# Kernel optimization log

Hardware: AMD Instinct MI355X
Metric: run time of the kernel (lower is better)

The kernel has to match this reference:

```python
import jax, jax.numpy as jnp
import numpy as np

B, SQ, SKV, D = 16, 2048, 2048, 128


def setup_inputs() -> dict:
    key = jax.random.key(0)
    kq, kk, kv = jax.random.split(key, 3)
    q = jax.random.normal(kq, (B, SQ, D), dtype=jnp.float32)
    k = jax.random.normal(kk, (B, SKV, D), dtype=jnp.float32)
    v = jax.random.normal(kv, (B, SKV, D), dtype=jnp.float32)
    return {"q": q, "k": k, "v": v, "dropout_p": 0}


def reference(q, k, v, dropout_p):
    # scores = q @ k^T, scaled by 1/sqrt(d)
    scale = 1.0 / np.sqrt(q.shape[-1]).astype(np.float32)
    scores = jnp.einsum('bqd,bkd->bqk', q, k) * scale  # [B, SQ, SKV]
    attn = jax.nn.softmax(scores, axis=-1)
    # dropout with p=dropout_p (0 here -> identity; deterministic baseline)
    if dropout_p > 0:
        keep = 1.0 - dropout_p
        mask = jax.random.bernoulli(jax.random.key(42), keep, attn.shape)
        attn = jnp.where(mask, attn / keep, 0.0)
    return jnp.einsum('bqk,bkd->bqd', attn, v)
```

## Files before the change

### kernel.cpp

```cpp
#include <hip/hip_runtime.h>
#include <hip/hip_bf16.h>
#include <cstdint>
#include <cmath>

#define SQL 2048
#define SKVL 2048
#define DD 128
#define NB 16
#define QBLK 32
#define KVB 32
#define NT (SKVL / KVB)

typedef __attribute__((ext_vector_type(8))) short short8;
typedef __attribute__((ext_vector_type(4))) float f32x4;

__device__ __forceinline__ ushort f2bf(float x) {
    union { float f; uint32_t u; } v; v.f = x;
    uint32_t r = v.u + 0x7FFFu + ((v.u >> 16) & 1u);
    return (ushort)(r >> 16);
}

__global__ void convert_scale_k(const float* __restrict__ in, ushort* __restrict__ out, float scale) {
    size_t i = (size_t)blockIdx.x * blockDim.x + threadIdx.x;
    const f32x4* p = (const f32x4*)in + i * 2;
    f32x4 a = p[0], b = p[1];
    short8 o;
    o[0] = (short)f2bf(a[0] * scale);
    o[1] = (short)f2bf(a[1] * scale);
    o[2] = (short)f2bf(a[2] * scale);
    o[3] = (short)f2bf(a[3] * scale);
    o[4] = (short)f2bf(b[0] * scale);
    o[5] = (short)f2bf(b[1] * scale);
    o[6] = (short)f2bf(b[2] * scale);
    o[7] = (short)f2bf(b[3] * scale);
    *((short8*)out + i) = o;
}

__global__ void convert_k_tiled(const float* __restrict__ in, ushort* __restrict__ out) {
    int gid = blockIdx.x * blockDim.x + threadIdx.x;
    int c16 = gid & 15;
    int rg  = gid >> 4;
    int r   = rg & 31;
    int tile = rg >> 5;
    const f32x4* p = (const f32x4*)(in + (size_t)rg * DD + c16 * 8);
    f32x4 a = p[0], b = p[1];
    short8 o;
    o[0] = (short)f2bf(a[0]); o[1] = (short)f2bf(a[1]);
    o[2] = (short)f2bf(a[2]); o[3] = (short)f2bf(a[3]);
    o[4] = (short)f2bf(b[0]); o[5] = (short)f2bf(b[1]);
    o[6] = (short)f2bf(b[2]); o[7] = (short)f2bf(b[3]);
    int cs = c16 ^ (r & 7);
    *(short8*)(out + ((size_t)tile << 12) + r * 128 + cs * 8) = o;
}

__global__ void convert_vt_tiled(const float* __restrict__ v, ushort* __restrict__ vt) {
    __shared__ float tile[32][129];
    int bid = blockIdx.x;
    int kt = bid & 63;
    int b  = bid >> 6;
    int tx = threadIdx.x;
    const float* src = v + ((size_t)b * SKVL + (size_t)kt * 32) * DD;
#pragma unroll
    for (int i = 0; i < 16; ++i) {
        int e = i * 256 + tx;
        tile[e >> 7][e & 127] = src[e];
    }
    __syncthreads();
    ushort* dst = vt + ((size_t)bid << 12);
#pragma unroll
    for (int i = 0; i < 2; ++i) {
        int q = i * 256 + tx;
        int d = q >> 2;
        int csp = q & 3;
        int cs = csp ^ ((d >> 1) & 3);
        short8 o;
#pragma unroll
        for (int j = 0; j < 8; ++j) {
            int kv = (j >> 2) * 16 + cs * 4 + (j & 3);
            o[j] = (short)f2bf(tile[kv][d]);
        }
        *(short8*)(dst + d * 32 + csp * 8) = o;
    }
}

#define GLD_LDS16(gsrc, ldst) \
    __builtin_amdgcn_global_load_lds((const __attribute__((address_space(1))) uint32_t*)(gsrc), \
                                     (__attribute__((address_space(3))) uint32_t*)(ldst), 16, 0, 0)

__global__ __launch_bounds__(128, 2) void fattn(
    const ushort* __restrict__ qb, const ushort* __restrict__ kbt,
    const ushort* __restrict__ vbt, float* __restrict__ out)
{
    __shared__ short8 kls[2][512];
    __shared__ short8 vls[2][512];

    int bid = blockIdx.x;
    int swz = (bid & 7) * 128 + (bid >> 3);
    int b  = swz >> 6;
    int qt = swz & 63;
    int lane = threadIdx.x & 63;
    int w = threadIdx.x >> 6;
    int g = lane >> 4;
    int qi = lane & 15;
    int rx = qi & 7;
    int vx = g ^ ((qi >> 1) & 3);
    int qrow = qt * QBLK + w * 16 + qi;

    const ushort* ktile0 = kbt + ((size_t)(b * NT) << 12);
    const ushort* vtile0 = vbt + ((size_t)(b * NT) << 12);

    const ushort* qptr = qb + ((size_t)b * SQL + qrow) * DD;
    short8 qf[4];
#pragma unroll
    for (int ks = 0; ks < 4; ++ks)
        qf[ks] = *(const short8*)(qptr + ks * 32 + g * 8);

    f32x4 acc[8];
#pragma unroll
    for (int i = 0; i < 8; ++i) acc[i] = (f32x4)0.f;
    float m = -1e30f, lsum = 0.f;

#pragma unroll
    for (int i = 0; i < 4; ++i) {
        int off = w * 4096 + i * 1024;
        GLD_LDS16((const char*)ktile0 + off + lane * 16, (char*)&kls[0][0] + off);
        GLD_LDS16((const char*)vtile0 + off + lane * 16, (char*)&vls[0][0] + off);
    }
    __syncthreads();

    for (int t = 0; t < NT; ++t) {
        int cur = t & 1, nxt = cur ^ 1;
        if (t + 1 < NT) {
            const char* ks = (const char*)ktile0 + ((size_t)(t + 1) << 13);
            const char* vs = (const char*)vtile0 + ((size_t)(t + 1) << 13);
#pragma unroll
            for (int i = 0; i < 4; ++i) {
                int off = w * 4096 + i * 1024;
                GLD_LDS16(ks + off + lane * 16, (char*)&kls[nxt][0] + off);
                GLD_LDS16(vs + off + lane * 16, (char*)&vls[nxt][0] + off);
            }
        }
        f32x4 st[2];
        __builtin_amdgcn_s_setprio(1);
#pragma unroll
        for (int sub = 0; sub < 2; ++sub) {
            f32x4 s = (f32x4)0.f;
            int r = sub * 16 + qi;
#pragma unroll
            for (int ks = 0; ks < 4; ++ks) {
                short8 kf = kls[cur][r * 16 + ((ks * 4 + g) ^ rx)];
                s = __builtin_amdgcn_mfma_f32_16x16x32_bf16(kf, qf[ks], s, 0, 0, 0);
            }
            st[sub] = s;
        }
        __builtin_amdgcn_s_setprio(0);
        float m0 = fmaxf(fmaxf(st[0][0], st[0][1]), fmaxf(st[0][2], st[0][3]));
        float m1 = fmaxf(fmaxf(st[1][0], st[1][1]), fmaxf(st[1][2], st[1][3]));
        float vmax = fmaxf(m0, m1);
        if (__any(vmax > m + 11.5f)) {
            float tmax = fmaxf(vmax, __shfl_xor(vmax, 16));
            tmax = fmaxf(tmax, __shfl_xor(tmax, 32));
            float mnew = fmaxf(m, tmax);
            float alpha = exp2f(m - mnew);
            m = mnew;
            lsum *= alpha;
#pragma unroll
            for (int i = 0; i < 8; ++i) {
                acc[i][0] *= alpha; acc[i][1] *= alpha;
                acc[i][2] *= alpha; acc[i][3] *= alpha;
            }
        }
        float pv[8];
#pragma unroll
        for (int s = 0; s < 2; ++s) {
            pv[s * 4 + 0] = exp2f(st[s][0] - m);
            pv[s * 4 + 1] = exp2f(st[s][1] - m);
            pv[s * 4 + 2] = exp2f(st[s][2] - m);
            pv[s * 4 + 3] = exp2f(st[s][3] - m);
        }
        lsum += ((pv[0] + pv[1]) + (pv[2] + pv[3])) + ((pv[4] + pv[5]) + (pv[6] + pv[7]));
        union { short8 v; uint32_t u[4]; } P;
#pragma unroll
        for (int i = 0; i < 4; ++i)
            asm("v_cvt_pk_bf16_f32 %0, %1, %2" : "=v"(P.u[i]) : "v"(pv[2 * i]), "v"(pv[2 * i + 1]));
        __builtin_amdgcn_s_setprio(1);
#pragma unroll
        for (int dt = 0; dt < 8; ++dt) {
            int d = dt * 16 + qi;
            acc[dt] = __builtin_amdgcn_mfma_f32_16x16x32_bf16(
                vls[cur][d * 4 + vx], P.v, acc[dt], 0, 0, 0);
        }
        __builtin_amdgcn_s_setprio(0);
        __syncthreads();
    }

    lsum += __shfl_xor(lsum, 16);
    lsum += __shfl_xor(lsum, 32);
    float inv = 1.f / lsum;
    float* optr = out + ((size_t)b * SQL + qrow) * DD + g * 4;
#pragma unroll
    for (int dt = 0; dt < 8; ++dt) {
        f32x4 o;
        o[0] = acc[dt][0] * inv; o[1] = acc[dt][1] * inv;
        o[2] = acc[dt][2] * inv; o[3] = acc[dt][3] * inv;
        *(f32x4*)(optr + dt * 16) = o;
    }
}

extern "C" void kernel_launch(void* const* d_in, const int* in_sizes, int n_in,
                              void* d_out, int out_size, void* d_ws, size_t ws_size,
                              hipStream_t stream) {
    const float* q = (const float*)d_in[0];
    const float* k = (const float*)d_in[1];
    const float* v = (const float*)d_in[2];
    float* out = (float*)d_out;

    uint8_t* w = (uint8_t*)d_ws;
    size_t tsz = (size_t)NB * SQL * DD * sizeof(ushort);
    ushort* qb  = (ushort*)w;
    ushort* kbt = (ushort*)(w + tsz);
    ushort* vbt = (ushort*)(w + 2 * tsz);

    float qscale = 1.4426950408889634f / sqrtf((float)DD);
    int n8 = NB * SQL * DD / 8;
    convert_scale_k<<<n8 / 256, 256, 0, stream>>>(q, qb, qscale);
    convert_k_tiled<<<NB * SKVL * 16 / 256, 256, 0, stream>>>(k, kbt);
    convert_vt_tiled<<<NB * (SKVL / 32), 256, 0, stream>>>(v, vbt);
    fattn<<<NB * (SQL / QBLK), 128, 0, stream>>>(qb, kbt, vbt, out);
}
```

Measured before the change: 164.2 us.

## Double query block per workgroup and split KV into two interleaved softmax streams

Each workgroup now handles 64 query rows with 4 waves, sharing each staged K/V tile across more waves to cut per-row global and LDS load traffic. The KV sequence is split into two halves processed in the same loop with separate running max, sum and accumulators, giving two independent MFMA/softmax chains per iteration and half as many iterations and barriers. The two partial results are merged with a log-sum-exp rescale at the end. This doubles accumulator registers, which may reduce occupancy.

```diff
diff --git a/kernel.cpp b/kernel.cpp
--- a/kernel.cpp
+++ b/kernel.cpp
@@ -7,9 +7,9 @@
 #define SKVL 2048
 #define DD 128
 #define NB 16
-#define QBLK 32
+#define QBLK 64
 #define KVB 32
-#define NT (SKVL / KVB)
+#define NT 32
 
 typedef __attribute__((ext_vector_type(8))) short short8;
 typedef __attribute__((ext_vector_type(4))) float f32x4;
@@ -87,17 +87,17 @@
     __builtin_amdgcn_global_load_lds((const __attribute__((address_space(1))) uint32_t*)(gsrc), \
                                      (__attribute__((address_space(3))) uint32_t*)(ldst), 16, 0, 0)
 
-__global__ __launch_bounds__(128, 2) void fattn(
+__global__ __launch_bounds__(256, 2) void fattn(
     const ushort* __restrict__ qb, const ushort* __restrict__ kbt,
     const ushort* __restrict__ vbt, float* __restrict__ out)
 {
-    __shared__ short8 kls[2][512];
-    __shared__ short8 vls[2][512];
+    __shared__ short8 kls[2][2][512];
+    __shared__ short8 vls[2][2][512];
 
     int bid = blockIdx.x;
-    int swz = (bid & 7) * 128 + (bid >> 3);
-    int b  = swz >> 6;
-    int qt = swz & 63;
+    int swz = (bid & 7) * 64 + (bid >> 3);
+    int b  = swz >> 5;
+    int qt = swz & 31;
     int lane = threadIdx.x & 63;
     int w = threadIdx.x >> 6;
     int g = lane >> 4;
@@ -106,8 +106,10 @@
     int vx = g ^ ((qi >> 1) & 3);
     int qrow = qt * QBLK + w * 16 + qi;
 
-    const ushort* ktile0 = kbt + ((size_t)(b * NT) << 12);
-    const ushort* vtile0 = vbt + ((size_t)(b * NT) << 12);
+    const char* kA = (const char*)(kbt + ((size_t)(b * 64) << 12));
+    const char* vA = (const char*)(vbt + ((size_t)(b * 64) << 12));
+    const char* kB = kA + ((size_t)NT << 13);
+    const char* vB = vA + ((size_t)NT << 13);
 
     const ushort* qptr = qb + ((size_t)b * SQL + qrow) * DD;
     short8 qf[4];
@@ -115,94 +117,109 @@
     for (int ks = 0; ks < 4; ++ks)
         qf[ks] = *(const short8*)(qptr + ks * 32 + g * 8);
 
-    f32x4 acc[8];
-#pragma unroll
-    for (int i = 0; i < 8; ++i) acc[i] = (f32x4)0.f;
-    float m = -1e30f, lsum = 0.f;
-
-#pragma unroll
-    for (int i = 0; i < 4; ++i) {
-        int off = w * 4096 + i * 1024;
-        GLD_LDS16((const char*)ktile0 + off + lane * 16, (char*)&kls[0][0] + off);
-        GLD_LDS16((const char*)vtile0 + off + lane * 16, (char*)&vls[0][0] + off);
+    f32x4 accA[8], accB[8];
+#pragma unroll
+    for (int i = 0; i < 8; ++i) { accA[i] = (f32x4)0.f; accB[i] = (f32x4)0.f; }
+    float mA = -1e30f, lA = 0.f, mB = -1e30f, lB = 0.f;
+
+#pragma unroll
+    for (int i = 0; i < 2; ++i) {
+        int off = w * 2048 + i * 1024;
+        GLD_LDS16(kA + off + lane * 16, (char*)&kls[0][0][0] + off);
+        GLD_LDS16(vA + off + lane * 16, (char*)&vls[0][0][0] + off);
+        GLD_LDS16(kB + off + lane * 16, (char*)&kls[1][0][0] + off);
+        GLD_LDS16(vB + off + lane * 16, (char*)&vls[1][0][0] + off);
     }
     __syncthreads();
 
     for (int t = 0; t < NT; ++t) {
         int cur = t & 1, nxt = cur ^ 1;
         if (t + 1 < NT) {
-            const char* ks = (const char*)ktile0 + ((size_t)(t + 1) << 13);
-            const char* vs = (const char*)vtile0 + ((size_t)(t + 1) << 13);
-#pragma unroll
-            for (int i = 0; i < 4; ++i) {
-                int off = w * 4096 + i * 1024;
-                GLD_LDS16(ks + off + lane * 16, (char*)&kls[nxt][0] + off);
-                GLD_LDS16(vs + off + lane * 16, (char*)&vls[nxt][0] + off);
+            size_t toff = (size_t)(t + 1) << 13;
+#pragma unroll
+            for (int i = 0; i < 2; ++i) {
+                int off = w * 2048 + i * 1024;
+                GLD_LDS16(kA + toff + off + lane * 16, (char*)&kls[0][nxt][0] + off);
+                GLD_LDS16(vA + toff + off + lane * 16, (char*)&vls[0][nxt][0] + off);
+                GLD_LDS16(kB + toff + off + lane * 16, (char*)&kls[1][nxt][0] + off);
+                GLD_LDS16(vB + toff + off + lane * 16, (char*)&vls[1][nxt][0] + off);
             }
         }
-        f32x4 st[2];
-        __builtin_amdgcn_s_setprio(1);
-#pragma unroll
-        for (int sub = 0; sub < 2; ++sub) {
-            f32x4 s = (f32x4)0.f;
-            int r = sub * 16 + qi;
-#pragma unroll
-            for (int ks = 0; ks < 4; ++ks) {
-                short8 kf = kls[cur][r * 16 + ((ks * 4 + g) ^ rx)];
-                s = __builtin_amdgcn_mfma_f32_16x16x32_bf16(kf, qf[ks], s, 0, 0, 0);
-            }
-            st[sub] = s;
+#pragma unroll
+        for (int s2 = 0; s2 < 2; ++s2) {
+            f32x4* acc = s2 ? accB : accA;
+            float& m = s2 ? mB : mA;
+            float& lsum = s2 ? lB : lA;
+            f32x4 st[2];
+            __builtin_amdgcn_s_setprio(1);
+#pragma unroll
+            for (int sub = 0; sub < 2; ++sub) {
+                f32x4 s = (f32x4)0.f;
+                int r = sub * 16 + qi;
+#pragma unroll
+                for (int ks = 0; ks < 4; ++ks) {
+                    short8 kf = kls[s2][cur][r * 16 + ((ks * 4 + g) ^ rx)];
+                    s = __builtin_amdgcn_mfma_f32_16x16x32_bf16(kf, qf[ks], s, 0, 0, 0);
+                }
+                st[sub] = s;
+            }
+            __builtin_amdgcn_s_setprio(0);
+            float m0 = fmaxf(fmaxf(st[0][0], st[0][1]), fmaxf(st[0][2], st[0][3]));
+            float m1 = fmaxf(fmaxf(st[1][0], st[1][1]), fmaxf(st[1][2], st[1][3]));
+            float vmax = fmaxf(m0, m1);
+            if (__any(vmax > m + 11.5f)) {
+                float tmax = fmaxf(vmax, __shfl_xor(vmax, 16));
+                tmax = fmaxf(tmax, __shfl_xor(tmax, 32));
+                float mnew = fmaxf(m, tmax);
+                float alpha = exp2f(m - mnew);
+                m = mnew;
+                lsum *= alpha;
+#pragma unroll
+                for (int i = 0; i < 8; ++i) {
+                    acc[i][0] *= alpha; acc[i][1] *= alpha;
+                    acc[i][2] *= alpha; acc[i][3] *= alpha;
+                }
+            }
+            float pvv[8];
+#pragma unroll
+            for (int s = 0; s < 2; ++s) {
+                pvv[s * 4 + 0] = exp2f(st[s][0] - m);
+                pvv[s * 4 + 1] = exp2f(st[s][1] - m);
+                pvv[s * 4 + 2] = exp2f(st[s][2] - m);
+                pvv[s * 4 + 3] = exp2f(st[s][3] - m);
+            }
+            lsum += ((pvv[0] + pvv[1]) + (pvv[2] + pvv[3])) + ((pvv[4] + pvv[5]) + (pvv[6] + pvv[7]));
+            union { short8 v; uint32_t u[4]; } P;
+#pragma unroll
+            for (int i = 0; i < 4; ++i)
+                asm("v_cvt_pk_bf16_f32 %0, %1, %2" : "=v"(P.u[i]) : "v"(pvv[2 * i]), "v"(pvv[2 * i + 1]));
+            __builtin_amdgcn_s_setprio(1);
+#pragma unroll
+            for (int dt = 0; dt < 8; ++dt) {
+                int d = dt * 16 + qi;
+                acc[dt] = __builtin_amdgcn_mfma_f32_16x16x32_bf16(
+                    vls[s2][cur][d * 4 + vx], P.v, acc[dt], 0, 0, 0);
+            }
+            __builtin_amdgcn_s_setprio(0);
         }
-        __builtin_amdgcn_s_setprio(0);
-        float m0 = fmaxf(fmaxf(st[0][0], st[0][1]), fmaxf(st[0][2], st[0][3]));
-        float m1 = fmaxf(fmaxf(st[1][0], st[1][1]), fmaxf(st[1][2], st[1][3]));
-        float vmax = fmaxf(m0, m1);
-        if (__any(vmax > m + 11.5f)) {
-            float tmax = fmaxf(vmax, __shfl_xor(vmax, 16));
-            tmax = fmaxf(tmax, __shfl_xor(tmax, 32));
-            float mnew = fmaxf(m, tmax);
-            float alpha = exp2f(m - mnew);
-            m = mnew;
-            lsum *= alpha;
-#pragma unroll
-            for (int i = 0; i < 8; ++i) {
-                acc[i][0] *= alpha; acc[i][1] *= alpha;
-                acc[i][2] *= alpha; acc[i][3] *= alpha;
-            }
-        }
-        float pv[8];
-#pragma unroll
-        for (int s = 0; s < 2; ++s) {
-            pv[s * 4 + 0] = exp2f(st[s][0] - m);
-            pv[s * 4 + 1] = exp2f(st[s][1] - m);
-            pv[s * 4 + 2] = exp2f(st[s][2] - m);
-            pv[s * 4 + 3] = exp2f(st[s][3] - m);
-        }
-        lsum += ((pv[0] + pv[1]) + (pv[2] + pv[3])) + ((pv[4] + pv[5]) + (pv[6] + pv[7]));
-        union { short8 v; uint32_t u[4]; } P;
-#pragma unroll
-        for (int i = 0; i < 4; ++i)
-            asm("v_cvt_pk_bf16_f32 %0, %1, %2" : "=v"(P.u[i]) : "v"(pv[2 * i]), "v"(pv[2 * i + 1]));
-        __builtin_amdgcn_s_setprio(1);
-#pragma unroll
-        for (int dt = 0; dt < 8; ++dt) {
-            int d = dt * 16 + qi;
-            acc[dt] = __builtin_amdgcn_mfma_f32_16x16x32_bf16(
-                vls[cur][d * 4 + vx], P.v, acc[dt], 0, 0, 0);
-        }
-        __builtin_amdgcn_s_setprio(0);
         __syncthreads();
     }
 
-    lsum += __shfl_xor(lsum, 16);
-    lsum += __shfl_xor(lsum, 32);
-    float inv = 1.f / lsum;
+    float mf = fmaxf(mA, mB);
+    float fa = exp2f(mA - mf), fb = exp2f(mB - mf);
+    float l = lA * fa + lB * fb;
+    l += __shfl_xor(l, 16);
+    l += __shfl_xor(l, 32);
+    float inv = 1.f / l;
+    float fia = fa * inv, fib = fb * inv;
     float* optr = out + ((size_t)b * SQL + qrow) * DD + g * 4;
 #pragma unroll
     for (int dt = 0; dt < 8; ++dt) {
         f32x4 o;
-        o[0] = acc[dt][0] * inv; o[1] = acc[dt][1] * inv;
-        o[2] = acc[dt][2] * inv; o[3] = acc[dt][3] * inv;
+        o[0] = accA[dt][0] * fia + accB[dt][0] * fib;
+        o[1] = accA[dt][1] * fia + accB[dt][1] * fib;
+        o[2] = accA[dt][2] * fia + accB[dt][2] * fib;
+        o[3] = accA[dt][3] * fia + accB[dt][3] * fib;
         *(f32x4*)(optr + dt * 16) = o;
     }
 }
@@ -226,5 +243,5 @@
     convert_scale_k<<<n8 / 256, 256, 0, stream>>>(q, qb, qscale);
     convert_k_tiled<<<NB * SKVL * 16 / 256, 256, 0, stream>>>(k, kbt);
     convert_vt_tiled<<<NB * (SKVL / 32), 256, 0, stream>>>(v, vbt);
-    fattn<<<NB * (SQL / QBLK), 128, 0, stream>>>(qb, kbt, vbt, out);
-}
+    fattn<<<NB * (SQL / QBLK), 256, 0, stream>>>(qb, kbt, vbt, out);
+}
```

Measured after the change: 155.8 us. -5.1%, faster.
